# Kernel tuning notes

Hardware: AMD Instinct MI355X
Metric: run time of the kernel (lower is better)

## Reference

```python
import jax, jax.numpy as jnp
import numpy as np

MIN_SUPPORT = 20.0
MAX_BEAR_ERROR = 20.0
AVG_ERROR = 0.05    # opt.cross_R_and_D_average_error
WEIGHT = 1.0        # opt.cross_weight_R_and_D


def setup_inputs() -> dict:
    key = jax.random.key(0)
    ks = jax.random.split(key, 14)
    bs, N, M, K, D = 16, 2048, 2048, 32, 128
    f32 = jnp.float32
    return {
        "r_tokens_full": jax.random.normal(ks[0], (bs, K, D), f32),
        "r_tokens_partial": jax.random.normal(ks[1], (bs, K, D), f32),
        "pc_seg_partial": jax.random.randint(ks[2], (bs, N, K), 0, 2).astype(f32),
        "pc_seg_full": jax.random.randint(ks[3], (bs, N, K), 0, 2).astype(f32),
        "pc_partial": jax.random.normal(ks[4], (bs, N, 3), f32),
        "deformed": jax.random.normal(ks[5], (bs, 3, M), f32),
        "p_rot": jax.random.normal(ks[6], (bs, 3, 3), f32),
        "p_t": jax.random.normal(ks[7], (bs, 1, 3), f32),
        "f_rot": jax.random.normal(ks[8], (bs, 3, 3), f32),
        "f_t": jax.random.normal(ks[9], (bs, 1, 3), f32),
        "tgt_rand_rot": jax.random.normal(ks[10], (bs, 3, 3), f32),
        "tgt_rand_t": jax.random.normal(ks[11], (bs, 1, 3), f32),
        "src_rand_rot": jax.random.normal(ks[12], (bs, 3, 3), f32),
        "src_rand_t": jax.random.normal(ks[13], (bs, 1, 3), f32),
    }


def reference(r_tokens_full, r_tokens_partial, pc_seg_partial, pc_seg_full,
              pc_partial, deformed, p_rot, p_t, f_rot, f_t,
              tgt_rand_rot, tgt_rand_t, src_rand_rot, src_rand_t):
    # --- get_cons_shape: chain of rigid transforms mapping partial pc into full frame
    z = jnp.matmul(pc_partial, p_rot) + p_t                       # [bs,N,3]
    z = jnp.matmul(z - tgt_rand_t, tgt_rand_rot.transpose(0, 2, 1))
    z = jnp.matmul(z, src_rand_rot) + src_rand_t
    x = jnp.matmul(z - f_t, f_rot.transpose(0, 2, 1))             # pc_partial_at_full [bs,N,3]

    # --- knn_points K=1: squared distance to nearest neighbor in deformed cloud
    y = deformed.transpose(0, 2, 1)                               # [bs,M,3]
    d2 = (jnp.sum(x * x, -1)[:, :, None]
          + jnp.sum(y * y, -1)[:, None, :]
          - 2.0 * jnp.einsum('bnd,bmd->bnm', x, y))               # [bs,N,M]
    cham_x = jnp.maximum(jnp.min(d2, axis=-1), 0.0)               # [bs,N]

    # seg^T @ cham: per-keypoint aggregated chamfer loss
    seg2def = jnp.einsum('bnk,bn->bk', pc_seg_partial, cham_x)    # [bs,K]

    sup_p = jnp.sum(pc_seg_partial, axis=1)                       # [bs,K]
    sup_f = jnp.sum(pc_seg_full, axis=1)                          # [bs,K]
    valid = (sup_p >= MIN_SUPPORT) & (sup_f >= MIN_SUPPORT)

    sp = jnp.maximum(sup_p, 1.0)
    sf = jnp.maximum(sup_f, 1.0)
    rel = jax.nn.sigmoid(seg2def / sp / AVG_ERROR)                # [bs,K]
    r_dis = jnp.sum((r_tokens_full / sf[..., None]
                     - r_tokens_partial / sp[..., None]) ** 2, axis=-1)
    loss_rd = (r_dis - rel) ** 2                                  # [bs,K]

    mask = valid & (loss_rd <= MAX_BEAR_ERROR)
    nofL = jnp.sum(mask).astype(loss_rd.dtype)
    total = jnp.sum(jnp.where(mask, loss_rd, 0.0))
    return total / (nofL + 1.0) * WEIGHT
```

## Files before the change

### kernel.cpp

```cpp
#include <hip/hip_runtime.h>
#include <math.h>

#define BS 16
#define NPTS 2048
#define MPTS 2048
#define KSEG 32
#define DDIM 128

#define ACC_TOTAL 0
#define ACC_COUNT 1
#define OFF_XFORM 16
#define OFF_SUPP 256
#define OFF_SUPF 768
#define OFF_S2D  1280
#define ZERO_REGION 2048
#define OFF_XN   2048
#define OFF_PART 34816

__global__ __launch_bounds__(256) void init_ws_kernel(
    const float* __restrict__ p_rot, const float* __restrict__ p_t,
    const float* __restrict__ f_rot, const float* __restrict__ f_t,
    const float* __restrict__ tg_rot, const float* __restrict__ tg_t,
    const float* __restrict__ sr_rot, const float* __restrict__ sr_t,
    float* __restrict__ ws)
{
    for (int i = threadIdx.x; i < ZERO_REGION; i += 256)
        if (i < OFF_XFORM || i >= OFF_XFORM + BS * 12) ws[i] = 0.0f;

    const int b = threadIdx.x;
    if (b < BS) {
        float P[9], F[9], Tg[9], Sr[9];
#pragma unroll
        for (int i = 0; i < 9; i++) {
            P[i] = p_rot[b*9+i];  F[i] = f_rot[b*9+i];
            Tg[i] = tg_rot[b*9+i]; Sr[i] = sr_rot[b*9+i];
        }
        float pt[3], ft[3], tt[3], st[3];
#pragma unroll
        for (int i = 0; i < 3; i++) {
            pt[i] = p_t[b*3+i]; ft[i] = f_t[b*3+i];
            tt[i] = tg_t[b*3+i]; st[i] = sr_t[b*3+i];
        }
        float A[9], Bm[9], R[9];
#pragma unroll
        for (int i = 0; i < 3; i++)
#pragma unroll
            for (int j = 0; j < 3; j++)
                A[i*3+j] = P[i*3+0]*Tg[j*3+0] + P[i*3+1]*Tg[j*3+1] + P[i*3+2]*Tg[j*3+2];
#pragma unroll
        for (int i = 0; i < 3; i++)
#pragma unroll
            for (int j = 0; j < 3; j++)
                Bm[i*3+j] = A[i*3+0]*Sr[0*3+j] + A[i*3+1]*Sr[1*3+j] + A[i*3+2]*Sr[2*3+j];
#pragma unroll
        for (int i = 0; i < 3; i++)
#pragma unroll
            for (int j = 0; j < 3; j++)
                R[i*3+j] = Bm[i*3+0]*F[j*3+0] + Bm[i*3+1]*F[j*3+1] + Bm[i*3+2]*F[j*3+2];
        float t0[3], t1[3], t2[3], t3[3], tv[3];
#pragma unroll
        for (int i = 0; i < 3; i++) t0[i] = pt[i] - tt[i];
#pragma unroll
        for (int j = 0; j < 3; j++)
            t1[j] = t0[0]*Tg[j*3+0] + t0[1]*Tg[j*3+1] + t0[2]*Tg[j*3+2];
#pragma unroll
        for (int j = 0; j < 3; j++)
            t2[j] = t1[0]*Sr[0*3+j] + t1[1]*Sr[1*3+j] + t1[2]*Sr[2*3+j];
#pragma unroll
        for (int i = 0; i < 3; i++) t3[i] = t2[i] + st[i] - ft[i];
#pragma unroll
        for (int j = 0; j < 3; j++)
            tv[j] = t3[0]*F[j*3+0] + t3[1]*F[j*3+1] + t3[2]*F[j*3+2];
        float* xf = ws + OFF_XFORM + b * 12;
#pragma unroll
        for (int i = 0; i < 9; i++) xf[i] = R[i];
#pragma unroll
        for (int i = 0; i < 3; i++) xf[9+i] = tv[i];
    }
}

__global__ __launch_bounds__(256) void cham_kernel(
    const float* __restrict__ pc_partial, const float* __restrict__ deformed,
    const float* __restrict__ ws_xf, float* __restrict__ xnArr,
    float* __restrict__ part)
{
    __shared__ float4 sh_y[256];
    __shared__ float pmin[4][512];

    const int bid  = blockIdx.x;
    const int b    = bid >> 5;
    const int r    = bid & 31;
    const int tile = r & 3;
    const int sg   = r >> 2;
    const int t = threadIdx.x;
    const int l = t & 63;
    const int w = t >> 6;

    const float* def0 = deformed + (size_t)b * 3 * MPTS + sg * 256;
    {
        float y0 = def0[t], y1 = def0[MPTS + t], y2 = def0[2*MPTS + t];
        sh_y[t] = make_float4(y0, y1, y2, 0.5f*(y0*y0 + y1*y1 + y2*y2));
    }

    const float* xf = ws_xf + b * 12;
    const float R00=xf[0],R01=xf[1],R02=xf[2],
                R10=xf[3],R11=xf[4],R12=xf[5],
                R20=xf[6],R21=xf[7],R22=xf[8],
                T0=xf[9],T1=xf[10],T2=xf[11];

    float x0[8], x1[8], x2[8], mn[8];
    const int nbase = tile * 512 + l;
    const float* pcb = pc_partial + (size_t)b * NPTS * 3;
#pragma unroll
    for (int j = 0; j < 8; j++) {
        const float* pc = pcb + (size_t)(nbase + 64*j) * 3;
        float px = pc[0], py = pc[1], pz = pc[2];
        x0[j] = px*R00 + py*R10 + pz*R20 + T0;
        x1[j] = px*R01 + py*R11 + pz*R21 + T1;
        x2[j] = px*R02 + py*R12 + pz*R22 + T2;
        mn[j] = 3.402823466e+38f;
    }
    if (sg == 0 && w == 0) {
#pragma unroll
        for (int j = 0; j < 8; j++)
            xnArr[(size_t)b*NPTS + nbase + 64*j] =
                x0[j]*x0[j] + x1[j]*x1[j] + x2[j]*x2[j];
    }
    __syncthreads();

    const int mb = w * 64;
#pragma unroll 4
    for (int i = 0; i < 64; i++) {
        float4 y = sh_y[mb + i];
#pragma unroll
        for (int j = 0; j < 8; j++) {
            float s = fmaf(-x2[j], y.z, fmaf(-x1[j], y.y, fmaf(-x0[j], y.x, y.w)));
            mn[j] = fminf(mn[j], s);
        }
    }

#pragma unroll
    for (int j = 0; j < 8; j++) pmin[w][64*j + l] = mn[j];
    __syncthreads();

#pragma unroll
    for (int u = 0; u < 2; u++) {
        int p = t + 256 * u;
        float v = fminf(fminf(pmin[0][p], pmin[1][p]),
                        fminf(pmin[2][p], pmin[3][p]));
        part[(size_t)sg * (BS*NPTS) + (size_t)b * NPTS + tile*512 + p] = v;
    }
}

__global__ __launch_bounds__(256) void seg_kernel(
    const float* __restrict__ seg_p, const float* __restrict__ seg_f,
    const float* __restrict__ xnArr, const float* __restrict__ part,
    float* __restrict__ ws)
{
    __shared__ float chamLDS[256];
    __shared__ float red[3][256];

    const int b = blockIdx.x >> 3;
    const int nc = blockIdx.x & 7;
    const int t = threadIdx.x;
    const int n0 = nc * 256;

    {
        const size_t nidx = (size_t)b * NPTS + n0 + t;
        float xn = xnArr[nidx];
        float pm = part[nidx];
#pragma unroll
        for (int sg = 1; sg < 8; sg++)
            pm = fminf(pm, part[(size_t)sg * (BS*NPTS) + nidx]);
        chamLDS[t] = fmaxf(fmaf(2.0f, pm, xn), 0.0f);
    }
    __syncthreads();

    const int k  = t & 31;
    const int ng = t >> 5;
    const float* sp = seg_p + ((size_t)b * NPTS + n0) * KSEG;
    const float* sf = seg_f + ((size_t)b * NPTS + n0) * KSEG;

    float ap = 0.f, af = 0.f, a2 = 0.f;
#pragma unroll 4
    for (int i = 0; i < 32; i++) {
        int n = ng + 8 * i;
        float c  = chamLDS[n];
        float vp = sp[n * KSEG + k];
        float vf = sf[n * KSEG + k];
        ap += vp;
        a2 += vp * c;
        af += vf;
    }
    red[0][t] = ap; red[1][t] = af; red[2][t] = a2;
    __syncthreads();
    if (t < KSEG) {
        float s0 = 0.f, s1 = 0.f, s2 = 0.f;
#pragma unroll
        for (int g = 0; g < 8; g++) {
            s0 += red[0][g*32 + t];
            s1 += red[1][g*32 + t];
            s2 += red[2][g*32 + t];
        }
        atomicAdd(&ws[OFF_SUPP + b*KSEG + t], s0);
        atomicAdd(&ws[OFF_SUPF + b*KSEG + t], s1);
        atomicAdd(&ws[OFF_S2D  + b*KSEG + t], s2);
    }
}

__global__ __launch_bounds__(256) void loss_kernel(
    const float* __restrict__ rf_tok, const float* __restrict__ rp_tok,
    float* __restrict__ ws)
{
    const int b  = blockIdx.x >> 1;
    const int kh = blockIdx.x & 1;
    const int t = threadIdx.x;
    const int cell = t >> 4;
    const int dg   = t & 15;
    const int k = kh * 16 + cell;

    const float supp = ws[OFF_SUPP + b*KSEG + k];
    const float supf = ws[OFF_SUPF + b*KSEG + k];
    const float s2d  = ws[OFF_S2D  + b*KSEG + k];
    const float spv = fmaxf(supp, 1.0f);
    const float sfv = fmaxf(supf, 1.0f);

    const float* rf = rf_tok + ((size_t)b * KSEG + k) * DDIM;
    const float* rp = rp_tok + ((size_t)b * KSEG + k) * DDIM;
    float acc = 0.f;
#pragma unroll
    for (int j = 0; j < 8; j++) {
        int d = dg + 16 * j;
        float v = rf[d] / sfv - rp[d] / spv;
        acc += v * v;
    }
#pragma unroll
    for (int off = 8; off; off >>= 1) acc += __shfl_xor(acc, off);

    __shared__ float lbuf[16], cbuf[16];
    if (dg == 0) {
        bool valid = (supp >= 20.0f) && (supf >= 20.0f);
        float arg = s2d / spv / 0.05f;
        float rel = 1.0f / (1.0f + expf(-arg));
        float ld = acc - rel; ld = ld * ld;
        bool msk = valid && (ld <= 20.0f);
        lbuf[cell] = msk ? ld : 0.0f;
        cbuf[cell] = msk ? 1.0f : 0.0f;
    }
    __syncthreads();
    if (t == 0) {
        float st = 0.f, sc = 0.f;
#pragma unroll
        for (int i = 0; i < 16; i++) { st += lbuf[i]; sc += cbuf[i]; }
        atomicAdd(&ws[ACC_TOTAL], st);
        atomicAdd(&ws[ACC_COUNT], sc);
    }
}

__global__ void final_kernel(const float* __restrict__ ws, float* __restrict__ out) {
    out[0] = ws[ACC_TOTAL] / (ws[ACC_COUNT] + 1.0f) * 1.0f;
}

extern "C" void kernel_launch(void* const* d_in, const int* in_sizes, int n_in,
                              void* d_out, int out_size, void* d_ws, size_t ws_size,
                              hipStream_t stream) {
    const float* r_tokens_full    = (const float*)d_in[0];
    const float* r_tokens_partial = (const float*)d_in[1];
    const float* pc_seg_partial   = (const float*)d_in[2];
    const float* pc_seg_full      = (const float*)d_in[3];
    const float* pc_partial       = (const float*)d_in[4];
    const float* deformed         = (const float*)d_in[5];
    const float* p_rot            = (const float*)d_in[6];
    const float* p_t              = (const float*)d_in[7];
    const float* f_rot            = (const float*)d_in[8];
    const float* f_t              = (const float*)d_in[9];
    const float* tgt_rand_rot     = (const float*)d_in[10];
    const float* tgt_rand_t       = (const float*)d_in[11];
    const float* src_rand_rot     = (const float*)d_in[12];
    const float* src_rand_t       = (const float*)d_in[13];

    float* ws  = (float*)d_ws;
    float* out = (float*)d_out;

    init_ws_kernel<<<1, 256, 0, stream>>>(
        p_rot, p_t, f_rot, f_t, tgt_rand_rot, tgt_rand_t,
        src_rand_rot, src_rand_t, ws);

    cham_kernel<<<BS * 32, 256, 0, stream>>>(
        pc_partial, deformed, ws + OFF_XFORM, ws + OFF_XN, ws + OFF_PART);

    seg_kernel<<<BS * 8, 256, 0, stream>>>(
        pc_seg_partial, pc_seg_full, ws + OFF_XN, ws + OFF_PART, ws);

    loss_kernel<<<BS * 2, 256, 0, stream>>>(r_tokens_full, r_tokens_partial, ws);

    final_kernel<<<1, 1, 0, stream>>>(ws, out);
}
```

Baseline: 103.2 us.

## Fuse transform setup into chamfer kernel, replace atomics with partials, vectorize seg loads

Removes the separate init kernel by recomputing the composed rigid transform in every chamfer block, so one launch and the workspace zeroing go away. The seg and loss kernels now write per-chunk partial sums to distinct workspace slots instead of using atomicAdd. The loss and final kernels reduce those partials, and the final kernel uses a wavefront shuffle. The seg kernel loads the segmentation masks as float4, which raises per-thread work and LDS reduction size.

```diff
diff --git a/kernel.cpp b/kernel.cpp
--- a/kernel.cpp
+++ b/kernel.cpp
@@ -7,82 +7,18 @@
 #define KSEG 32
 #define DDIM 128
 
-#define ACC_TOTAL 0
-#define ACC_COUNT 1
-#define OFF_XFORM 16
-#define OFF_SUPP 256
-#define OFF_SUPF 768
-#define OFF_S2D  1280
-#define ZERO_REGION 2048
-#define OFF_XN   2048
-#define OFF_PART 34816
-
-__global__ __launch_bounds__(256) void init_ws_kernel(
+#define OFF_XN    0
+#define OFF_PART  32768
+#define OFF_SEGP  294912
+#define OFF_LOSSP 307200
+
+__global__ __launch_bounds__(256) void cham_kernel(
+    const float* __restrict__ pc_partial, const float* __restrict__ deformed,
     const float* __restrict__ p_rot, const float* __restrict__ p_t,
     const float* __restrict__ f_rot, const float* __restrict__ f_t,
     const float* __restrict__ tg_rot, const float* __restrict__ tg_t,
     const float* __restrict__ sr_rot, const float* __restrict__ sr_t,
-    float* __restrict__ ws)
-{
-    for (int i = threadIdx.x; i < ZERO_REGION; i += 256)
-        if (i < OFF_XFORM || i >= OFF_XFORM + BS * 12) ws[i] = 0.0f;
-
-    const int b = threadIdx.x;
-    if (b < BS) {
-        float P[9], F[9], Tg[9], Sr[9];
-#pragma unroll
-        for (int i = 0; i < 9; i++) {
-            P[i] = p_rot[b*9+i];  F[i] = f_rot[b*9+i];
-            Tg[i] = tg_rot[b*9+i]; Sr[i] = sr_rot[b*9+i];
-        }
-        float pt[3], ft[3], tt[3], st[3];
-#pragma unroll
-        for (int i = 0; i < 3; i++) {
-            pt[i] = p_t[b*3+i]; ft[i] = f_t[b*3+i];
-            tt[i] = tg_t[b*3+i]; st[i] = sr_t[b*3+i];
-        }
-        float A[9], Bm[9], R[9];
-#pragma unroll
-        for (int i = 0; i < 3; i++)
-#pragma unroll
-            for (int j = 0; j < 3; j++)
-                A[i*3+j] = P[i*3+0]*Tg[j*3+0] + P[i*3+1]*Tg[j*3+1] + P[i*3+2]*Tg[j*3+2];
-#pragma unroll
-        for (int i = 0; i < 3; i++)
-#pragma unroll
-            for (int j = 0; j < 3; j++)
-                Bm[i*3+j] = A[i*3+0]*Sr[0*3+j] + A[i*3+1]*Sr[1*3+j] + A[i*3+2]*Sr[2*3+j];
-#pragma unroll
-        for (int i = 0; i < 3; i++)
-#pragma unroll
-            for (int j = 0; j < 3; j++)
-                R[i*3+j] = Bm[i*3+0]*F[j*3+0] + Bm[i*3+1]*F[j*3+1] + Bm[i*3+2]*F[j*3+2];
-        float t0[3], t1[3], t2[3], t3[3], tv[3];
-#pragma unroll
-        for (int i = 0; i < 3; i++) t0[i] = pt[i] - tt[i];
-#pragma unroll
-        for (int j = 0; j < 3; j++)
-            t1[j] = t0[0]*Tg[j*3+0] + t0[1]*Tg[j*3+1] + t0[2]*Tg[j*3+2];
-#pragma unroll
-        for (int j = 0; j < 3; j++)
-            t2[j] = t1[0]*Sr[0*3+j] + t1[1]*Sr[1*3+j] + t1[2]*Sr[2*3+j];
-#pragma unroll
-        for (int i = 0; i < 3; i++) t3[i] = t2[i] + st[i] - ft[i];
-#pragma unroll
-        for (int j = 0; j < 3; j++)
-            tv[j] = t3[0]*F[j*3+0] + t3[1]*F[j*3+1] + t3[2]*F[j*3+2];
-        float* xf = ws + OFF_XFORM + b * 12;
-#pragma unroll
-        for (int i = 0; i < 9; i++) xf[i] = R[i];
-#pragma unroll
-        for (int i = 0; i < 3; i++) xf[9+i] = tv[i];
-    }
-}
-
-__global__ __launch_bounds__(256) void cham_kernel(
-    const float* __restrict__ pc_partial, const float* __restrict__ deformed,
-    const float* __restrict__ ws_xf, float* __restrict__ xnArr,
-    float* __restrict__ part)
+    float* __restrict__ xnArr, float* __restrict__ part)
 {
     __shared__ float4 sh_y[256];
     __shared__ float pmin[4][512];
@@ -102,11 +38,45 @@
         sh_y[t] = make_float4(y0, y1, y2, 0.5f*(y0*y0 + y1*y1 + y2*y2));
     }
 
-    const float* xf = ws_xf + b * 12;
-    const float R00=xf[0],R01=xf[1],R02=xf[2],
-                R10=xf[3],R11=xf[4],R12=xf[5],
-                R20=xf[6],R21=xf[7],R22=xf[8],
-                T0=xf[9],T1=xf[10],T2=xf[11];
+    float R[9], T[3];
+    {
+        float P[9], F[9], Tg[9], Sr[9];
+#pragma unroll
+        for (int i = 0; i < 9; i++) {
+            P[i] = p_rot[b*9+i];  F[i] = f_rot[b*9+i];
+            Tg[i] = tg_rot[b*9+i]; Sr[i] = sr_rot[b*9+i];
+        }
+        float A[9], Bm[9];
+#pragma unroll
+        for (int i = 0; i < 3; i++)
+#pragma unroll
+            for (int j = 0; j < 3; j++)
+                A[i*3+j] = P[i*3+0]*Tg[j*3+0] + P[i*3+1]*Tg[j*3+1] + P[i*3+2]*Tg[j*3+2];
+#pragma unroll
+        for (int i = 0; i < 3; i++)
+#pragma unroll
+            for (int j = 0; j < 3; j++)
+                Bm[i*3+j] = A[i*3+0]*Sr[0*3+j] + A[i*3+1]*Sr[1*3+j] + A[i*3+2]*Sr[2*3+j];
+#pragma unroll
+        for (int i = 0; i < 3; i++)
+#pragma unroll
+            for (int j = 0; j < 3; j++)
+                R[i*3+j] = Bm[i*3+0]*F[j*3+0] + Bm[i*3+1]*F[j*3+1] + Bm[i*3+2]*F[j*3+2];
+        float t0[3], t1[3], t2[3], t3[3];
+#pragma unroll
+        for (int i = 0; i < 3; i++) t0[i] = p_t[b*3+i] - tg_t[b*3+i];
+#pragma unroll
+        for (int j = 0; j < 3; j++)
+            t1[j] = t0[0]*Tg[j*3+0] + t0[1]*Tg[j*3+1] + t0[2]*Tg[j*3+2];
+#pragma unroll
+        for (int j = 0; j < 3; j++)
+            t2[j] = t1[0]*Sr[0*3+j] + t1[1]*Sr[1*3+j] + t1[2]*Sr[2*3+j];
+#pragma unroll
+        for (int i = 0; i < 3; i++) t3[i] = t2[i] + sr_t[b*3+i] - f_t[b*3+i];
+#pragma unroll
+        for (int j = 0; j < 3; j++)
+            T[j] = t3[0]*F[j*3+0] + t3[1]*F[j*3+1] + t3[2]*F[j*3+2];
+    }
 
     float x0[8], x1[8], x2[8], mn[8];
     const int nbase = tile * 512 + l;
@@ -115,9 +85,9 @@
     for (int j = 0; j < 8; j++) {
         const float* pc = pcb + (size_t)(nbase + 64*j) * 3;
         float px = pc[0], py = pc[1], pz = pc[2];
-        x0[j] = px*R00 + py*R10 + pz*R20 + T0;
-        x1[j] = px*R01 + py*R11 + pz*R21 + T1;
-        x2[j] = px*R02 + py*R12 + pz*R22 + T2;
+        x0[j] = px*R[0] + py*R[3] + pz*R[6] + T[0];
+        x1[j] = px*R[1] + py*R[4] + pz*R[7] + T[1];
+        x2[j] = px*R[2] + py*R[5] + pz*R[8] + T[2];
         mn[j] = 3.402823466e+38f;
     }
     if (sg == 0 && w == 0) {
@@ -158,7 +128,7 @@
     float* __restrict__ ws)
 {
     __shared__ float chamLDS[256];
-    __shared__ float red[3][256];
+    __shared__ float red0[1024], red1[1024], red2[1024];
 
     const int b = blockIdx.x >> 3;
     const int nc = blockIdx.x & 7;
@@ -176,35 +146,43 @@
     }
     __syncthreads();
 
-    const int k  = t & 31;
-    const int ng = t >> 5;
-    const float* sp = seg_p + ((size_t)b * NPTS + n0) * KSEG;
-    const float* sf = seg_f + ((size_t)b * NPTS + n0) * KSEG;
-
-    float ap = 0.f, af = 0.f, a2 = 0.f;
-#pragma unroll 4
-    for (int i = 0; i < 32; i++) {
-        int n = ng + 8 * i;
-        float c  = chamLDS[n];
-        float vp = sp[n * KSEG + k];
-        float vf = sf[n * KSEG + k];
-        ap += vp;
-        a2 += vp * c;
-        af += vf;
-    }
-    red[0][t] = ap; red[1][t] = af; red[2][t] = a2;
-    __syncthreads();
+    const int l = t & 63;
+    const int w = t >> 6;
+    const int rowoff = l >> 3;
+    const int k4 = l & 7;
+    const float4* sp4 = (const float4*)(seg_p + ((size_t)b * NPTS + n0) * KSEG);
+    const float4* sf4 = (const float4*)(seg_f + ((size_t)b * NPTS + n0) * KSEG);
+
+    float4 ap = make_float4(0.f,0.f,0.f,0.f);
+    float4 af = make_float4(0.f,0.f,0.f,0.f);
+    float4 a2 = make_float4(0.f,0.f,0.f,0.f);
+#pragma unroll
+    for (int i = 0; i < 8; i++) {
+        int n = w * 64 + i * 8 + rowoff;
+        float c = chamLDS[n];
+        float4 vp = sp4[n * 8 + k4];
+        float4 vf = sf4[n * 8 + k4];
+        ap.x += vp.x; ap.y += vp.y; ap.z += vp.z; ap.w += vp.w;
+        af.x += vf.x; af.y += vf.y; af.z += vf.z; af.w += vf.w;
+        a2.x = fmaf(vp.x, c, a2.x); a2.y = fmaf(vp.y, c, a2.y);
+        a2.z = fmaf(vp.z, c, a2.z); a2.w = fmaf(vp.w, c, a2.w);
+    }
+    red0[t*4+0] = ap.x; red0[t*4+1] = ap.y; red0[t*4+2] = ap.z; red0[t*4+3] = ap.w;
+    red1[t*4+0] = af.x; red1[t*4+1] = af.y; red1[t*4+2] = af.z; red1[t*4+3] = af.w;
+    red2[t*4+0] = a2.x; red2[t*4+1] = a2.y; red2[t*4+2] = a2.z; red2[t*4+3] = a2.w;
+    __syncthreads();
+
     if (t < KSEG) {
         float s0 = 0.f, s1 = 0.f, s2 = 0.f;
 #pragma unroll
-        for (int g = 0; g < 8; g++) {
-            s0 += red[0][g*32 + t];
-            s1 += red[1][g*32 + t];
-            s2 += red[2][g*32 + t];
+        for (int j = 0; j < 32; j++) {
+            s0 += red0[j*32 + t];
+            s1 += red1[j*32 + t];
+            s2 += red2[j*32 + t];
         }
-        atomicAdd(&ws[OFF_SUPP + b*KSEG + t], s0);
-        atomicAdd(&ws[OFF_SUPF + b*KSEG + t], s1);
-        atomicAdd(&ws[OFF_S2D  + b*KSEG + t], s2);
+        ws[OFF_SEGP + ((0*BS + b)*8 + nc)*KSEG + t] = s0;
+        ws[OFF_SEGP + ((1*BS + b)*8 + nc)*KSEG + t] = s1;
+        ws[OFF_SEGP + ((2*BS + b)*8 + nc)*KSEG + t] = s2;
     }
 }
 
@@ -219,9 +197,12 @@
     const int dg   = t & 15;
     const int k = kh * 16 + cell;
 
-    const float supp = ws[OFF_SUPP + b*KSEG + k];
-    const float supf = ws[OFF_SUPF + b*KSEG + k];
-    const float s2d  = ws[OFF_S2D  + b*KSEG + k];
+    float supp = 0.f, supf = 0.f;
+#pragma unroll
+    for (int nc = 0; nc < 8; nc++) {
+        supp += ws[OFF_SEGP + ((0*BS + b)*8 + nc)*KSEG + k];
+        supf += ws[OFF_SEGP + ((1*BS + b)*8 + nc)*KSEG + k];
+    }
     const float spv = fmaxf(supp, 1.0f);
     const float sfv = fmaxf(supf, 1.0f);
 
@@ -239,6 +220,10 @@
 
     __shared__ float lbuf[16], cbuf[16];
     if (dg == 0) {
+        float s2d = 0.f;
+#pragma unroll
+        for (int nc = 0; nc < 8; nc++)
+            s2d += ws[OFF_SEGP + ((2*BS + b)*8 + nc)*KSEG + k];
         bool valid = (supp >= 20.0f) && (supf >= 20.0f);
         float arg = s2d / spv / 0.05f;
         float rel = 1.0f / (1.0f + expf(-arg));
@@ -252,13 +237,23 @@
         float st = 0.f, sc = 0.f;
 #pragma unroll
         for (int i = 0; i < 16; i++) { st += lbuf[i]; sc += cbuf[i]; }
-        atomicAdd(&ws[ACC_TOTAL], st);
-        atomicAdd(&ws[ACC_COUNT], sc);
-    }
-}
-
-__global__ void final_kernel(const float* __restrict__ ws, float* __restrict__ out) {
-    out[0] = ws[ACC_TOTAL] / (ws[ACC_COUNT] + 1.0f) * 1.0f;
+        ws[OFF_LOSSP + blockIdx.x]      = st;
+        ws[OFF_LOSSP + 32 + blockIdx.x] = sc;
+    }
+}
+
+__global__ __launch_bounds__(64) void final_kernel(
+    const float* __restrict__ ws, float* __restrict__ out)
+{
+    const int t = threadIdx.x;
+    float v1 = (t < 32) ? ws[OFF_LOSSP + t] : 0.0f;
+    float v2 = (t < 32) ? ws[OFF_LOSSP + 32 + t] : 0.0f;
+#pragma unroll
+    for (int off = 16; off; off >>= 1) {
+        v1 += __shfl_xor(v1, off);
+        v2 += __shfl_xor(v2, off);
+    }
+    if (t == 0) out[0] = v1 / (v2 + 1.0f) * 1.0f;
 }
 
 extern "C" void kernel_launch(void* const* d_in, const int* in_sizes, int n_in,
@@ -282,17 +277,15 @@
     float* ws  = (float*)d_ws;
     float* out = (float*)d_out;
 
-    init_ws_kernel<<<1, 256, 0, stream>>>(
-        p_rot, p_t, f_rot, f_t, tgt_rand_rot, tgt_rand_t,
-        src_rand_rot, src_rand_t, ws);
-
     cham_kernel<<<BS * 32, 256, 0, stream>>>(
-        pc_partial, deformed, ws + OFF_XFORM, ws + OFF_XN, ws + OFF_PART);
+        pc_partial, deformed, p_rot, p_t, f_rot, f_t,
+        tgt_rand_rot, tgt_rand_t, src_rand_rot, src_rand_t,
+        ws + OFF_XN, ws + OFF_PART);
 
     seg_kernel<<<BS * 8, 256, 0, stream>>>(
         pc_seg_partial, pc_seg_full, ws + OFF_XN, ws + OFF_PART, ws);
 
     loss_kernel<<<BS * 2, 256, 0, stream>>>(r_tokens_full, r_tokens_partial, ws);
 
-    final_kernel<<<1, 1, 0, stream>>>(ws, out);
-}
+    final_kernel<<<1, 64, 0, stream>>>(ws, out);
+}
```

After: 100.00 us. -3.1%, faster.
